# Kernel tuning notes

Measured on AMD Instinct MI355X. Metric: run time of the kernel, lower is better.

Reference implementation:

```python
import jax, jax.numpy as jnp
import numpy as np

EMBED_DIM = 1024
NUM_HEADS = 16
HEAD_DIM = EMBED_DIM // NUM_HEADS
SCALE = HEAD_DIM ** -0.5


def setup_inputs() -> dict:
    key = jax.random.key(0)
    k_x, k_wqkv, k_bqkv, k_wp, k_bp = jax.random.split(key, 5)
    B, N = 2, 2048
    x = jax.random.normal(k_x, (B, N, EMBED_DIM), dtype=jnp.float32)
    # torch.nn.Linear default init: U(-1/sqrt(fan_in), 1/sqrt(fan_in))
    lim = 1.0 / np.sqrt(EMBED_DIM)
    W_qkv = jax.random.uniform(k_wqkv, (EMBED_DIM, 3 * EMBED_DIM), jnp.float32, -lim, lim)
    b_qkv = jax.random.uniform(k_bqkv, (3 * EMBED_DIM,), jnp.float32, -lim, lim)
    W_proj = jax.random.uniform(k_wp, (EMBED_DIM, EMBED_DIM), jnp.float32, -lim, lim)
    b_proj = jax.random.uniform(k_bp, (EMBED_DIM,), jnp.float32, -lim, lim)
    return {"x": x, "W_qkv": W_qkv, "b_qkv": b_qkv, "W_proj": W_proj, "b_proj": b_proj}


def reference(x, W_qkv, b_qkv, W_proj, b_proj):
    B, N, C = x.shape
    qkv = x @ W_qkv + b_qkv                              # [B, N, 3C]
    qkv = qkv.reshape(B, N, 3, NUM_HEADS, HEAD_DIM)
    qkv = jnp.transpose(qkv, (2, 0, 3, 1, 4))            # [3, B, H, N, D]
    q, k, v = qkv[0], qkv[1], qkv[2]
    attn = jnp.einsum('bhnd,bhmd->bhnm', q, k) * SCALE   # [B, H, N, N]
    attn = jax.nn.softmax(attn, axis=-1)
    out = jnp.einsum('bhnm,bhmd->bhnd', attn, v)         # [B, H, N, D]
    out = jnp.transpose(out, (0, 2, 1, 3)).reshape(B, N, C)
    return out @ W_proj + b_proj
```

## Files before the change

### kernel.cpp

```cpp
#include <hip/hip_runtime.h>
#include <math.h>

typedef unsigned short u16;
typedef _Float16 f16;
typedef f16 f16x8 __attribute__((ext_vector_type(8)));
typedef __fp16 hp16x2 __attribute__((ext_vector_type(2)));
typedef float f32x4 __attribute__((ext_vector_type(4)));
typedef float f32x16 __attribute__((ext_vector_type(16)));

#define SEQ   2048
#define NH    16
#define HD    64
#define EMB   1024
#define NQKV  3072
#define BATCH 2
#define QSCALE 0.18033688f

__device__ __forceinline__ u16 f2h(float f) {
  union { f16 h; u16 u; } w; w.h = (f16)f; return w.u;
}

__device__ __forceinline__ void gload16(const void* g, void* l) {
  __builtin_amdgcn_global_load_lds(
      (const __attribute__((address_space(1))) unsigned int*)g,
      (__attribute__((address_space(3))) unsigned int*)l, 16, 0, 0);
}

__global__ __launch_bounds__(256) void cvt_x(const float* __restrict__ X,
                                             u16* __restrict__ Xh) {
  const size_t i = ((size_t)blockIdx.x * 256 + threadIdx.x) * 8;
  float4 a = *reinterpret_cast<const float4*>(&X[i]);
  float4 b = *reinterpret_cast<const float4*>(&X[i + 4]);
  union { hp16x2 h2[4]; float4 f; } pk;
  pk.h2[0] = __builtin_amdgcn_cvt_pkrtz(a.x, a.y);
  pk.h2[1] = __builtin_amdgcn_cvt_pkrtz(a.z, a.w);
  pk.h2[2] = __builtin_amdgcn_cvt_pkrtz(b.x, b.y);
  pk.h2[3] = __builtin_amdgcn_cvt_pkrtz(b.z, b.w);
  *reinterpret_cast<float4*>(&Xh[i]) = pk.f;
}

__global__ __launch_bounds__(256) void cvt_wt(const float* __restrict__ W,
                                              u16* __restrict__ Wt,
                                              int K, int N) {
  __shared__ u16 T[64][68];
  const int n0 = blockIdx.x << 6, k0 = blockIdx.y << 6;
  const int t = threadIdx.x;
  const int rr = t >> 4, cc = (t & 15) << 2;
#pragma unroll
  for (int p = 0; p < 4; p++) {
    const int kr = p * 16 + rr;
    float4 v = *reinterpret_cast<const float4*>(&W[(size_t)(k0 + kr) * N + n0 + cc]);
    T[cc + 0][kr] = f2h(v.x); T[cc + 1][kr] = f2h(v.y);
    T[cc + 2][kr] = f2h(v.z); T[cc + 3][kr] = f2h(v.w);
  }
  __syncthreads();
#pragma unroll
  for (int p = 0; p < 4; p++) {
    const int nr = p * 16 + rr;
    union { u16 s[4]; unsigned long long d; } o;
    o.s[0] = T[nr][cc + 0]; o.s[1] = T[nr][cc + 1];
    o.s[2] = T[nr][cc + 2]; o.s[3] = T[nr][cc + 3];
    *reinterpret_cast<unsigned long long*>(&Wt[(size_t)(n0 + nr) * K + k0 + cc]) = o.d;
  }
}

__device__ __forceinline__ void gemm_core(const u16* __restrict__ Ag,
                                          const u16* __restrict__ Bg,
                                          int m0, int n0, int t,
                                          f32x4 acc[4][4]) {
  __shared__ __align__(16) u16 As[128 * 32];
  __shared__ __align__(16) u16 Bs[128 * 32];
  const int lane = t & 63, w = t >> 6;
  const int l15  = lane & 15, quad = lane >> 4;
  const int wm = w >> 1, wn = w & 1;
  const int srow  = lane >> 2;
  const int gslot = (lane & 3) ^ ((srow >> 1) & 3);
  const int xk    = (quad ^ ((l15 >> 1) & 3)) << 3;

  for (int k0 = 0; k0 < EMB; k0 += 32) {
    __syncthreads();
#pragma unroll
    for (int i = 0; i < 2; i++) {
      const int ca = w * 2 + i;
      const int arow = ca * 16 + srow;
      gload16(Ag + (size_t)(m0 + arow) * EMB + k0 + gslot * 8, &As[ca * 512]);
      gload16(Bg + (size_t)(n0 + arow) * EMB + k0 + gslot * 8, &Bs[ca * 512]);
    }
    __syncthreads();
    f16x8 af[4], bf[4];
#pragma unroll
    for (int s = 0; s < 4; s++)
      af[s] = *reinterpret_cast<const f16x8*>(&As[(wm * 64 + s * 16 + l15) * 32 + xk]);
#pragma unroll
    for (int s = 0; s < 4; s++)
      bf[s] = *reinterpret_cast<const f16x8*>(&Bs[(wn * 64 + s * 16 + l15) * 32 + xk]);
#pragma unroll
    for (int i = 0; i < 4; i++)
#pragma unroll
      for (int j = 0; j < 4; j++)
        acc[i][j] = __builtin_amdgcn_mfma_f32_16x16x32_f16(af[i], bf[j], acc[i][j], 0, 0, 0);
  }
}

__global__ __launch_bounds__(256) void k_qkv(const u16* __restrict__ Ag,
                                             const u16* __restrict__ Bg,
                                             const float* __restrict__ bias,
                                             u16* __restrict__ qo,
                                             u16* __restrict__ ko,
                                             u16* __restrict__ vo) {
  const int t = threadIdx.x;
  const int lane = t & 63, w = t >> 6;
  const int l15 = lane & 15, quad = lane >> 4;
  const int wm = w >> 1, wn = w & 1;
  const int m0 = blockIdx.y << 7, n0 = blockIdx.x << 7;
  f32x4 acc[4][4];
#pragma unroll
  for (int i = 0; i < 4; i++)
#pragma unroll
    for (int j = 0; j < 4; j++) acc[i][j] = (f32x4){0.f, 0.f, 0.f, 0.f};
  gemm_core(Ag, Bg, m0, n0, t, acc);
#pragma unroll
  for (int j = 0; j < 4; j++) {
    const int c = n0 + wn * 64 + j * 16 + l15;
    const int which = c >> 10, h = (c >> 6) & 15, d = c & 63;
    const float bv = bias[c];
    const float sc = (which == 0) ? QSCALE : 1.0f;
#pragma unroll
    for (int i = 0; i < 4; i++) {
#pragma unroll
      for (int r = 0; r < 4; r++) {
        const int m  = m0 + wm * 64 + i * 16 + quad * 4 + r;
        const int bb = m >> 11, n = m & (SEQ - 1);
        const u16 val = f2h((acc[i][j][r] + bv) * sc);
        if (which == 2)
          vo[(((size_t)bb * NH + h) * HD + d) * SEQ + n] = val;
        else if (which == 1)
          ko[((((size_t)bb * NH + h) * SEQ) + n) * HD + d] = val;
        else
          qo[((((size_t)bb * NH + h) * SEQ) + n) * HD + d] = val;
      }
    }
  }
}

__global__ __launch_bounds__(256) void k_proj(const u16* __restrict__ Ag,
                                              const u16* __restrict__ Bg,
                                              const float* __restrict__ bias,
                                              float* __restrict__ out) {
  const int t = threadIdx.x;
  const int lane = t & 63, w = t >> 6;
  const int l15 = lane & 15, quad = lane >> 4;
  const int wm = w >> 1, wn = w & 1;
  const int m0 = blockIdx.y << 7, n0 = blockIdx.x << 7;
  f32x4 acc[4][4];
#pragma unroll
  for (int i = 0; i < 4; i++)
#pragma unroll
    for (int j = 0; j < 4; j++) acc[i][j] = (f32x4){0.f, 0.f, 0.f, 0.f};
  gemm_core(Ag, Bg, m0, n0, t, acc);
#pragma unroll
  for (int j = 0; j < 4; j++) {
    const int c = n0 + wn * 64 + j * 16 + l15;
    const float bv = bias[c];
#pragma unroll
    for (int i = 0; i < 4; i++) {
#pragma unroll
      for (int r = 0; r < 4; r++) {
        const int m = m0 + wm * 64 + i * 16 + quad * 4 + r;
        out[(size_t)m * EMB + c] = acc[i][j][r] + bv;
      }
    }
  }
}

__global__ __launch_bounds__(512, 4) void k_attn(const u16* __restrict__ Qg,
                                                 const u16* __restrict__ Kg,
                                                 const u16* __restrict__ Vtg,
                                                 u16* __restrict__ AO) {
  __shared__ __align__(16) u16 KV[2][2][2][64 * 64];
  __shared__ float Lx[256];
  const int t    = threadIdx.x;
  const int lane = t & 63, w = t >> 6;
  const int grp  = w >> 2, wl = w & 3;
  const int l31  = lane & 31, hi = lane >> 5;
  const int bh   = blockIdx.y;
  const int q0   = blockIdx.x << 7;
  const size_t base = (size_t)bh * SEQ * HD;

  f16x8 qf[4];
  {
    const u16* qp = Qg + base + (size_t)(q0 + 32 * wl + l31) * HD + hi * 8;
#pragma unroll
    for (int c = 0; c < 4; c++) {
      union { float4 f; f16x8 v; } fu;
      fu.f = *reinterpret_cast<const float4*>(qp + c * 16);
      qf[c] = fu.v;
    }
  }

  f32x16 O0 = {}, O1 = {};
  float lsum = 0.f;
  const int fsw = (l31 >> 1) & 7;
  const int srw = lane >> 3, ssl = lane & 7;
  const int kbeg = grp << 10;
  const int kend = kbeg + (SEQ / 2);

  auto STAGE = [&](int buf, int kt) {
    u16* Ksb = KV[buf][grp][0];
    u16* Vsb = KV[buf][grp][1];
#pragma unroll
    for (int i = 0; i < 2; i++) {
      const int ca  = wl * 2 + i;
      const int row = ca * 8 + srw;
      const int sg  = (ssl ^ ((row >> 1) & 7)) << 3;
      gload16(Kg  + base + (size_t)(kt + row) * HD + sg, &Ksb[ca * 512]);
      gload16(Vtg + base + (size_t)row * SEQ + kt + sg,  &Vsb[ca * 512]);
    }
  };

  STAGE(0, kbeg);
  __syncthreads();

  int cur = 0;
  for (int kt = kbeg; kt < kend; kt += 64) {
    if (kt + 64 < kend) STAGE(cur ^ 1, kt + 64);
    const u16* Ks = KV[cur][grp][0];
    const u16* Vs = KV[cur][grp][1];

#pragma unroll
    for (int sk = 0; sk < 2; sk++) {
      f32x16 c = {};
#pragma unroll
      for (int cc = 0; cc < 4; cc++) {
        f16x8 kf = *reinterpret_cast<const f16x8*>(
            &Ks[(sk * 32 + l31) * 64 + (((cc * 2 + hi) ^ fsw) << 3)]);
        c = __builtin_amdgcn_mfma_f32_32x32x16_f16(kf, qf[cc], c, 0, 0, 0);
      }
      unsigned pw[4][2];
#pragma unroll
      for (int g = 0; g < 4; g++) {
        const float p0 = exp2f(c[4 * g + 0]);
        const float p1 = exp2f(c[4 * g + 1]);
        const float p2 = exp2f(c[4 * g + 2]);
        const float p3 = exp2f(c[4 * g + 3]);
        lsum += (p0 + p1) + (p2 + p3);
        union { hp16x2 h; unsigned u; } w0, w1;
        w0.h = __builtin_amdgcn_cvt_pkrtz(p0, p1);
        w1.h = __builtin_amdgcn_cvt_pkrtz(p2, p3);
        pw[g][0] = w0.u; pw[g][1] = w1.u;
      }
#pragma unroll
      for (int s = 0; s < 2; s++) {
        const unsigned a0 = pw[2 * s][0],     a1 = pw[2 * s][1];
        const unsigned b0 = pw[2 * s + 1][0], b1 = pw[2 * s + 1][1];
        const unsigned x0 = (unsigned)__shfl_xor((int)(hi ? a0 : b0), 32);
        const unsigned x1 = (unsigned)__shfl_xor((int)(hi ? a1 : b1), 32);
        union { unsigned u[4]; f16x8 v; } fr;
        fr.u[0] = hi ? x0 : a0;
        fr.u[1] = hi ? x1 : a1;
        fr.u[2] = hi ? b0 : x0;
        fr.u[3] = hi ? b1 : x1;
        const int cc = sk * 2 + s;
        f16x8 vf0 = *reinterpret_cast<const f16x8*>(
            &Vs[l31 * 64 + (((cc * 2 + hi) ^ fsw) << 3)]);
        f16x8 vf1 = *reinterpret_cast<const f16x8*>(
            &Vs[(32 + l31) * 64 + (((cc * 2 + hi) ^ fsw) << 3)]);
        O0 = __builtin_amdgcn_mfma_f32_32x32x16_f16(fr.v, vf0, O0, 0, 0, 0);
        O1 = __builtin_amdgcn_mfma_f32_32x32x16_f16(fr.v, vf1, O1, 0, 0, 0);
      }
    }
    __syncthreads();
    cur ^= 1;
  }

  float* Xch = reinterpret_cast<float*>(&KV[0][0][0][0]);
  const int li = wl * 64 + lane;
  if (grp == 1) {
#pragma unroll
    for (int g4 = 0; g4 < 4; g4++) {
      f32x4 v0 = { O0[4 * g4 + 0], O0[4 * g4 + 1], O0[4 * g4 + 2], O0[4 * g4 + 3] };
      *reinterpret_cast<f32x4*>(&Xch[(g4 * 256 + li) * 4]) = v0;
      f32x4 v1 = { O1[4 * g4 + 0], O1[4 * g4 + 1], O1[4 * g4 + 2], O1[4 * g4 + 3] };
      *reinterpret_cast<f32x4*>(&Xch[((4 + g4) * 256 + li) * 4]) = v1;
    }
    Lx[li] = lsum;
  }
  __syncthreads();
  if (grp == 0) {
#pragma unroll
    for (int g4 = 0; g4 < 4; g4++) {
      f32x4 v0 = *reinterpret_cast<const f32x4*>(&Xch[(g4 * 256 + li) * 4]);
      f32x4 v1 = *reinterpret_cast<const f32x4*>(&Xch[((4 + g4) * 256 + li) * 4]);
#pragma unroll
      for (int j = 0; j < 4; j++) {
        O0[4 * g4 + j] += v0[j];
        O1[4 * g4 + j] += v1[j];
      }
    }
    lsum += Lx[li];
    lsum += __shfl_xor(lsum, 32);
    const int b = bh >> 4, h = bh & 15;
#pragma unroll
    for (int g = 0; g < 4; g++) {
#pragma unroll
      for (int rr = 0; rr < 4; rr++) {
        const int r = g * 4 + rr;
        const int qrow = rr + 8 * g + 4 * hi;
        const float inv = 1.f / __shfl(lsum, qrow, 64);
        const int n = q0 + 32 * wl + qrow;
        u16* dst = AO + ((size_t)(b * SEQ + n)) * EMB + h * HD;
        dst[l31]      = f2h(O0[r] * inv);
        dst[32 + l31] = f2h(O1[r] * inv);
      }
    }
  }
}

extern "C" void kernel_launch(void* const* d_in, const int* in_sizes, int n_in,
                              void* d_out, int out_size, void* d_ws, size_t ws_size,
                              hipStream_t stream) {
  (void)in_sizes; (void)n_in; (void)out_size; (void)ws_size;
  const float* x     = (const float*)d_in[0];
  const float* Wqkv  = (const float*)d_in[1];
  const float* bqkv  = (const float*)d_in[2];
  const float* Wproj = (const float*)d_in[3];
  const float* bproj = (const float*)d_in[4];
  float* out = (float*)d_out;

  const size_t NE = (size_t)BATCH * SEQ * EMB;
  u16* q    = (u16*)d_ws;
  u16* k    = q + NE;
  u16* vt   = k + NE;
  u16* aoxh = vt + NE;
  u16* Wt   = aoxh + NE;
  u16* Wpt  = Wt + (size_t)NQKV * EMB;

  cvt_x<<<NE / 2048, 256, 0, stream>>>(x, aoxh);
  dim3 gw1(NQKV / 64, EMB / 64);
  cvt_wt<<<gw1, 256, 0, stream>>>(Wqkv, Wt, EMB, NQKV);
  dim3 gw2(EMB / 64, EMB / 64);
  cvt_wt<<<gw2, 256, 0, stream>>>(Wproj, Wpt, EMB, EMB);

  dim3 gq(NQKV / 128, (BATCH * SEQ) / 128);
  k_qkv<<<gq, 256, 0, stream>>>(aoxh, Wt, bqkv, q, k, vt);

  dim3 ga(SEQ / 128, BATCH * NH);
  k_attn<<<ga, 512, 0, stream>>>(q, k, vt, aoxh);

  dim3 gp(EMB / 128, (BATCH * SEQ) / 128);
  k_proj<<<gp, 256, 0, stream>>>(aoxh, Wpt, bproj, out);
}
```

Baseline: 207.8 us.

## Swizzle attention block order, raise MFMA priority, use permlane32 swap and native exp2

Several micro-optimizations to the attention kernel. Block IDs are remapped so that consecutive blocks spread across heads, which may improve L2/XCD locality. s_setprio raises wave priority around the MFMA sections so they interleave better with softmax work. The two-shuffle plus select exchange of P fragments is replaced with v_permlane32_swap. exp2f is replaced with the raw hardware exp2 builtin, which drops denormal and range handling. The exact lane semantics of permlane32_swap must match the old select logic, or the output will be wrong.

```diff
diff --git a/kernel.cpp b/kernel.cpp
--- a/kernel.cpp
+++ b/kernel.cpp
@@ -7,6 +7,7 @@
 typedef __fp16 hp16x2 __attribute__((ext_vector_type(2)));
 typedef float f32x4 __attribute__((ext_vector_type(4)));
 typedef float f32x16 __attribute__((ext_vector_type(16)));
+typedef unsigned u32x2 __attribute__((ext_vector_type(2)));
 
 #define SEQ   2048
 #define NH    16
@@ -183,8 +184,10 @@
   const int lane = t & 63, w = t >> 6;
   const int grp  = w >> 2, wl = w & 3;
   const int l31  = lane & 31, hi = lane >> 5;
-  const int bh   = blockIdx.y;
-  const int q0   = blockIdx.x << 7;
+  const int id   = blockIdx.y * 16 + blockIdx.x;
+  const int swz  = ((id & 7) << 6) | (id >> 3);
+  const int bh   = swz >> 4;
+  const int q0   = (swz & 15) << 7;
   const size_t base = (size_t)bh * SEQ * HD;
 
   f16x8 qf[4];
@@ -230,36 +233,39 @@
 #pragma unroll
     for (int sk = 0; sk < 2; sk++) {
       f32x16 c = {};
+      __builtin_amdgcn_s_setprio(1);
 #pragma unroll
       for (int cc = 0; cc < 4; cc++) {
         f16x8 kf = *reinterpret_cast<const f16x8*>(
             &Ks[(sk * 32 + l31) * 64 + (((cc * 2 + hi) ^ fsw) << 3)]);
         c = __builtin_amdgcn_mfma_f32_32x32x16_f16(kf, qf[cc], c, 0, 0, 0);
       }
+      __builtin_amdgcn_s_setprio(0);
       unsigned pw[4][2];
 #pragma unroll
       for (int g = 0; g < 4; g++) {
-        const float p0 = exp2f(c[4 * g + 0]);
-        const float p1 = exp2f(c[4 * g + 1]);
-        const float p2 = exp2f(c[4 * g + 2]);
-        const float p3 = exp2f(c[4 * g + 3]);
+        const float p0 = __builtin_amdgcn_exp2f(c[4 * g + 0]);
+        const float p1 = __builtin_amdgcn_exp2f(c[4 * g + 1]);
+        const float p2 = __builtin_amdgcn_exp2f(c[4 * g + 2]);
+        const float p3 = __builtin_amdgcn_exp2f(c[4 * g + 3]);
         lsum += (p0 + p1) + (p2 + p3);
         union { hp16x2 h; unsigned u; } w0, w1;
         w0.h = __builtin_amdgcn_cvt_pkrtz(p0, p1);
         w1.h = __builtin_amdgcn_cvt_pkrtz(p2, p3);
         pw[g][0] = w0.u; pw[g][1] = w1.u;
       }
+      __builtin_amdgcn_s_setprio(1);
 #pragma unroll
       for (int s = 0; s < 2; s++) {
-        const unsigned a0 = pw[2 * s][0],     a1 = pw[2 * s][1];
-        const unsigned b0 = pw[2 * s + 1][0], b1 = pw[2 * s + 1][1];
-        const unsigned x0 = (unsigned)__shfl_xor((int)(hi ? a0 : b0), 32);
-        const unsigned x1 = (unsigned)__shfl_xor((int)(hi ? a1 : b1), 32);
+        u32x2 r02 = __builtin_amdgcn_permlane32_swap(
+            pw[2 * s][0], pw[2 * s + 1][0], false, false);
+        u32x2 r13 = __builtin_amdgcn_permlane32_swap(
+            pw[2 * s][1], pw[2 * s + 1][1], false, false);
         union { unsigned u[4]; f16x8 v; } fr;
-        fr.u[0] = hi ? x0 : a0;
-        fr.u[1] = hi ? x1 : a1;
-        fr.u[2] = hi ? b0 : x0;
-        fr.u[3] = hi ? b1 : x1;
+        fr.u[0] = r02.x;
+        fr.u[1] = r13.x;
+        fr.u[2] = r02.y;
+        fr.u[3] = r13.y;
         const int cc = sk * 2 + s;
         f16x8 vf0 = *reinterpret_cast<const f16x8*>(
             &Vs[l31 * 64 + (((cc * 2 + hi) ^ fsw) << 3)]);
@@ -268,6 +274,7 @@
         O0 = __builtin_amdgcn_mfma_f32_32x32x16_f16(fr.v, vf0, O0, 0, 0, 0);
         O1 = __builtin_amdgcn_mfma_f32_32x32x16_f16(fr.v, vf1, O1, 0, 0, 0);
       }
+      __builtin_amdgcn_s_setprio(0);
     }
     __syncthreads();
     cur ^= 1;
```

After: 193.7 us. -6.8%, faster.
